# Optimization experiments

Hardware: AMD Instinct MI355X
Metric: run time of the kernel (lower is better)

## Reference

```python
import jax, jax.numpy as jnp
import numpy as np

B, T, D = 128, 1024, 128

def setup_inputs() -> dict:
    key = jax.random.key(0)
    k1, k2 = jax.random.split(key)
    x = jax.random.normal(k1, (B, T, 3 * D), dtype=jnp.float32)
    # original init: kernel = gain * eye(d_dim); use eye plus small noise for a nontrivial test
    kernel = jnp.eye(D, dtype=jnp.float32) + 0.01 * jax.random.normal(k2, (D, D), dtype=jnp.float32)
    return {"x": x, "kernel": kernel}

def reference(x, kernel):
    d = kernel.shape[0]
    # x: (B, T, 3d) -> channel blocks (module permutes to (B,C,T) then back; net effect is slicing last dim)
    y = x[:, :, :d]            # (B, T, d) observed values
    w = x[:, :, d:2 * d]       # (B, T, d) log-intensities
    y_obs = x[:, :, 2 * d:3 * d]  # (B, T, d) transient targets
    intensity = jnp.exp(w)
    # softmax across channels per timestep (exp(w - logsumexp_d w))
    sm = jax.nn.softmax(w, axis=2)
    mean = jnp.mean(y, axis=1, keepdims=True)  # (B, 1, d), broadcast over T
    # cross-channel mixing: small per-timestep d x d matmul
    smooth = jnp.matmul(sm * (y - mean), kernel) + mean  # (B, T, d)
    y_trans = y_obs - smooth
    # concat order matches torch.cat([rep1, intensity, y_trans], dim=1) after final permute
    return jnp.concatenate([smooth, intensity, y_trans], axis=-1)  # (B, T, 3d)
```

## Files before the change

### kernel.cpp

```cpp
#include <hip/hip_runtime.h>
#include <cstdint>

#define D_CH 128
#define T_LEN 1024
#define ROWLEN 384
#define NROWS (128 * 1024)
#define TILE 64
#define NCHUNK (NROWS / TILE)
#define VSTR_B 272
#define VS_SLICE (16 * VSTR_B)
#define EPI_W 132
#define EPI_SLICE (16 * EPI_W * 4)

typedef __attribute__((ext_vector_type(8))) _Float16 f16x8;
typedef __attribute__((ext_vector_type(4))) _Float16 f16x4;
typedef __attribute__((ext_vector_type(4))) float f32x4;

__global__ __launch_bounds__(256) void prep_kernel(const float* __restrict__ x,
                                                   const float* __restrict__ Kmat,
                                                   float* __restrict__ meang,
                                                   _Float16* __restrict__ Ktg) {
  int bid = blockIdx.x;
  int b = bid >> 1, h = bid & 1;
  int tid = threadIdx.x;
  int li = tid & 15, tt = tid >> 4;
  int d4 = h * 64 + 4 * li;
  float4 s = make_float4(0.f, 0.f, 0.f, 0.f);
  const float* xp = x + (size_t)b * T_LEN * ROWLEN + d4;
#pragma unroll 4
  for (int j = 0; j < 64; ++j) {
    int t = tt + 16 * j;
    float4 v = *(const float4*)(xp + (size_t)t * ROWLEN);
    s.x += v.x; s.y += v.y; s.z += v.z; s.w += v.w;
  }
  __shared__ float4 red[16][17];
  red[tt][li] = s;
  __syncthreads();
  for (int st = 8; st > 0; st >>= 1) {
    if (tt < st) {
      float4 o = red[tt + st][li];
      float4 m = red[tt][li];
      m.x += o.x; m.y += o.y; m.z += o.z; m.w += o.w;
      red[tt][li] = m;
    }
    __syncthreads();
  }
  if (tt == 0) {
    float4 m = red[0][li];
    const float inv = 1.0f / 1024.0f;
    m.x *= inv; m.y *= inv; m.z *= inv; m.w *= inv;
    *(float4*)(meang + b * D_CH + d4) = m;
  }
  if (tid < 64) {
    int f = bid * 64 + tid;
    int j = f & 7;
    int lane = (f >> 3) & 63;
    int q = f >> 9;
    int ks = q & 3, nt = q >> 2;
    int kk = ks * 32 + (lane >> 4) * 8 + j;
    int nn = nt * 16 + (lane & 15);
    Ktg[f] = (_Float16)Kmat[kk * D_CH + nn];
  }
}

__global__ __launch_bounds__(256, 3) void main_kernel(const float* __restrict__ x,
                                                      const float* __restrict__ meang,
                                                      const _Float16* __restrict__ Ktg,
                                                      float* __restrict__ out) {
  __shared__ alignas(16) char vsbuf[4 * VS_SLICE];
  __shared__ alignas(16) char epibuf[4 * EPI_SLICE];
  int tid = threadIdx.x;
  int wave = tid >> 6, lane = tid & 63;
  int hf = lane >> 5, li = lane & 31;
  int c0 = 4 * li;
  int m0 = wave * 16;
  int l15 = lane & 15, lg = lane >> 4;
  char* vslice = vsbuf + wave * VS_SLICE;
  float* epi = (float*)(epibuf + wave * EPI_SLICE);

  int chunk = blockIdx.x;
  int row0 = chunk * TILE;
  int bb = chunk >> 4;
  const float* mb = meang + bb * D_CH;
  float4 mn = *(const float4*)(mb + c0);

  float4 yb[8], wb[8];
#pragma unroll
  for (int i = 0; i < 8; ++i) {
    size_t base = (size_t)(row0 + m0 + 2 * i + hf) * ROWLEN + c0;
    yb[i] = *(const float4*)(x + base);
    wb[i] = *(const float4*)(x + base + 128);
  }
#pragma unroll
  for (int i = 0; i < 8; ++i) {
    int lr = 2 * i + hf;
    int row = row0 + m0 + lr;
    float4 e;
    e.x = __expf(wb[i].x); e.y = __expf(wb[i].y);
    e.z = __expf(wb[i].z); e.w = __expf(wb[i].w);
    *(float4*)(out + (size_t)row * ROWLEN + 128 + c0) = e;
    float s = e.x + e.y + e.z + e.w;
    s += __shfl_xor(s, 1, 32);
    s += __shfl_xor(s, 2, 32);
    s += __shfl_xor(s, 4, 32);
    s += __shfl_xor(s, 8, 32);
    s += __shfl_xor(s, 16, 32);
    float rinv = 1.0f / s;
    f16x4 vh;
    vh[0] = (_Float16)(e.x * rinv * (yb[i].x - mn.x));
    vh[1] = (_Float16)(e.y * rinv * (yb[i].y - mn.y));
    vh[2] = (_Float16)(e.z * rinv * (yb[i].z - mn.z));
    vh[3] = (_Float16)(e.w * rinv * (yb[i].w - mn.w));
    *(f16x4*)(vslice + lr * VSTR_B + li * 8) = vh;
  }

  f16x8 a[4];
#pragma unroll
  for (int ks = 0; ks < 4; ++ks)
    a[ks] = *(const f16x8*)(vslice + l15 * VSTR_B + ks * 64 + lg * 16);
  f32x4 acc[8];
#pragma unroll
  for (int nt = 0; nt < 8; ++nt) {
    acc[nt] = (f32x4){0.f, 0.f, 0.f, 0.f};
#pragma unroll
    for (int ks = 0; ks < 4; ++ks) {
      f16x8 bf = *(const f16x8*)&Ktg[((nt * 4 + ks) * 64 + lane) * 8];
      acc[nt] = __builtin_amdgcn_mfma_f32_16x16x32_f16(a[ks], bf, acc[nt], 0, 0, 0);
    }
  }

#pragma unroll
  for (int nt = 0; nt < 8; ++nt)
#pragma unroll
    for (int r = 0; r < 4; ++r)
      epi[(lg * 4 + r) * EPI_W + nt * 16 + l15] = acc[nt][r];

#pragma unroll
  for (int i = 0; i < 8; ++i) {
    int lr = 2 * i + hf;
    size_t ob = (size_t)(row0 + m0 + lr) * ROWLEN;
    float4 sm4 = *(const float4*)&epi[lr * EPI_W + c0];
    sm4.x += mn.x; sm4.y += mn.y; sm4.z += mn.z; sm4.w += mn.w;
    float4 yo = *(const float4*)(x + ob + 256 + c0);
    *(float4*)(out + ob + c0) = sm4;
    float4 yt;
    yt.x = yo.x - sm4.x; yt.y = yo.y - sm4.y;
    yt.z = yo.z - sm4.z; yt.w = yo.w - sm4.w;
    *(float4*)(out + ob + 256 + c0) = yt;
  }
}

extern "C" void kernel_launch(void* const* d_in, const int* in_sizes, int n_in,
                              void* d_out, int out_size, void* d_ws, size_t ws_size,
                              hipStream_t stream) {
  const float* x = (const float*)d_in[0];
  const float* Kmat = (const float*)d_in[1];
  float* out = (float*)d_out;
  float* meang = (float*)d_ws;
  _Float16* Ktg = (_Float16*)((char*)d_ws + 65536);
  prep_kernel<<<256, 256, 0, stream>>>(x, Kmat, meang, Ktg);
  main_kernel<<<NCHUNK, 256, 0, stream>>>(x, meang, Ktg, out);
}
```

Baseline: 350.2 us.

## Alias LDS buffers, use nontemporal global access, widen prep reduction blocks

The main kernel now reuses one per-wave LDS slice for both the fp16 MFMA operand staging and the fp32 epilogue buffer. This cuts shared memory per block, and the launch bound goes from 3 to 4 blocks per CU to take advantage of it. All streaming loads of x and stores to out use nontemporal builtins, to avoid polluting the cache with data that is touched only once. The prep kernel moves to 1024 threads per block with a deeper tree reduction, so each thread does fewer serial loads for the mean. The aliasing relies on in-wave LDS ordering, since there is no barrier between the last operand read and the first epilogue write.

```diff
diff --git a/kernel.cpp b/kernel.cpp
--- a/kernel.cpp
+++ b/kernel.cpp
@@ -8,48 +8,40 @@
 #define TILE 64
 #define NCHUNK (NROWS / TILE)
 #define VSTR_B 272
-#define VS_SLICE (16 * VSTR_B)
 #define EPI_W 132
-#define EPI_SLICE (16 * EPI_W * 4)
+#define SLICE_B 8448
 
 typedef __attribute__((ext_vector_type(8))) _Float16 f16x8;
 typedef __attribute__((ext_vector_type(4))) _Float16 f16x4;
 typedef __attribute__((ext_vector_type(4))) float f32x4;
 
-__global__ __launch_bounds__(256) void prep_kernel(const float* __restrict__ x,
-                                                   const float* __restrict__ Kmat,
-                                                   float* __restrict__ meang,
-                                                   _Float16* __restrict__ Ktg) {
+__global__ __launch_bounds__(1024) void prep_kernel(const float* __restrict__ x,
+                                                    const float* __restrict__ Kmat,
+                                                    float* __restrict__ meang,
+                                                    _Float16* __restrict__ Ktg) {
   int bid = blockIdx.x;
   int b = bid >> 1, h = bid & 1;
   int tid = threadIdx.x;
   int li = tid & 15, tt = tid >> 4;
   int d4 = h * 64 + 4 * li;
-  float4 s = make_float4(0.f, 0.f, 0.f, 0.f);
+  f32x4 s = {0.f, 0.f, 0.f, 0.f};
   const float* xp = x + (size_t)b * T_LEN * ROWLEN + d4;
 #pragma unroll 4
-  for (int j = 0; j < 64; ++j) {
-    int t = tt + 16 * j;
-    float4 v = *(const float4*)(xp + (size_t)t * ROWLEN);
-    s.x += v.x; s.y += v.y; s.z += v.z; s.w += v.w;
+  for (int j = 0; j < 16; ++j) {
+    int t = tt + 64 * j;
+    f32x4 v = *(const f32x4*)(xp + (size_t)t * ROWLEN);
+    s += v;
   }
-  __shared__ float4 red[16][17];
+  __shared__ f32x4 red[64][17];
   red[tt][li] = s;
   __syncthreads();
-  for (int st = 8; st > 0; st >>= 1) {
-    if (tt < st) {
-      float4 o = red[tt + st][li];
-      float4 m = red[tt][li];
-      m.x += o.x; m.y += o.y; m.z += o.z; m.w += o.w;
-      red[tt][li] = m;
-    }
+  for (int st = 32; st > 0; st >>= 1) {
+    if (tt < st) red[tt][li] += red[tt + st][li];
     __syncthreads();
   }
   if (tt == 0) {
-    float4 m = red[0][li];
-    const float inv = 1.0f / 1024.0f;
-    m.x *= inv; m.y *= inv; m.z *= inv; m.w *= inv;
-    *(float4*)(meang + b * D_CH + d4) = m;
+    f32x4 m = red[0][li] * (1.0f / 1024.0f);
+    *(f32x4*)(meang + b * D_CH + d4) = m;
   }
   if (tid < 64) {
     int f = bid * 64 + tid;
@@ -63,43 +55,42 @@
   }
 }
 
-__global__ __launch_bounds__(256, 3) void main_kernel(const float* __restrict__ x,
+__global__ __launch_bounds__(256, 4) void main_kernel(const float* __restrict__ x,
                                                       const float* __restrict__ meang,
                                                       const _Float16* __restrict__ Ktg,
                                                       float* __restrict__ out) {
-  __shared__ alignas(16) char vsbuf[4 * VS_SLICE];
-  __shared__ alignas(16) char epibuf[4 * EPI_SLICE];
+  __shared__ alignas(16) char smem[4 * SLICE_B];
   int tid = threadIdx.x;
   int wave = tid >> 6, lane = tid & 63;
   int hf = lane >> 5, li = lane & 31;
   int c0 = 4 * li;
   int m0 = wave * 16;
   int l15 = lane & 15, lg = lane >> 4;
-  char* vslice = vsbuf + wave * VS_SLICE;
-  float* epi = (float*)(epibuf + wave * EPI_SLICE);
+  char* vslice = smem + wave * SLICE_B;
+  float* epi = (float*)(smem + wave * SLICE_B);
 
   int chunk = blockIdx.x;
   int row0 = chunk * TILE;
   int bb = chunk >> 4;
   const float* mb = meang + bb * D_CH;
-  float4 mn = *(const float4*)(mb + c0);
+  f32x4 mn = *(const f32x4*)(mb + c0);
 
-  float4 yb[8], wb[8];
+  f32x4 yb[8], wb[8];
 #pragma unroll
   for (int i = 0; i < 8; ++i) {
     size_t base = (size_t)(row0 + m0 + 2 * i + hf) * ROWLEN + c0;
-    yb[i] = *(const float4*)(x + base);
-    wb[i] = *(const float4*)(x + base + 128);
+    yb[i] = __builtin_nontemporal_load((const f32x4*)(x + base));
+    wb[i] = __builtin_nontemporal_load((const f32x4*)(x + base + 128));
   }
 #pragma unroll
   for (int i = 0; i < 8; ++i) {
     int lr = 2 * i + hf;
     int row = row0 + m0 + lr;
-    float4 e;
-    e.x = __expf(wb[i].x); e.y = __expf(wb[i].y);
-    e.z = __expf(wb[i].z); e.w = __expf(wb[i].w);
-    *(float4*)(out + (size_t)row * ROWLEN + 128 + c0) = e;
-    float s = e.x + e.y + e.z + e.w;
+    f32x4 e;
+    e[0] = __expf(wb[i][0]); e[1] = __expf(wb[i][1]);
+    e[2] = __expf(wb[i][2]); e[3] = __expf(wb[i][3]);
+    __builtin_nontemporal_store(e, (f32x4*)(out + (size_t)row * ROWLEN + 128 + c0));
+    float s = e[0] + e[1] + e[2] + e[3];
     s += __shfl_xor(s, 1, 32);
     s += __shfl_xor(s, 2, 32);
     s += __shfl_xor(s, 4, 32);
@@ -107,10 +98,10 @@
     s += __shfl_xor(s, 16, 32);
     float rinv = 1.0f / s;
     f16x4 vh;
-    vh[0] = (_Float16)(e.x * rinv * (yb[i].x - mn.x));
-    vh[1] = (_Float16)(e.y * rinv * (yb[i].y - mn.y));
-    vh[2] = (_Float16)(e.z * rinv * (yb[i].z - mn.z));
-    vh[3] = (_Float16)(e.w * rinv * (yb[i].w - mn.w));
+    vh[0] = (_Float16)(e[0] * rinv * (yb[i][0] - mn[0]));
+    vh[1] = (_Float16)(e[1] * rinv * (yb[i][1] - mn[1]));
+    vh[2] = (_Float16)(e[2] * rinv * (yb[i][2] - mn[2]));
+    vh[3] = (_Float16)(e[3] * rinv * (yb[i][3] - mn[3]));
     *(f16x4*)(vslice + lr * VSTR_B + li * 8) = vh;
   }
 
@@ -139,14 +130,12 @@
   for (int i = 0; i < 8; ++i) {
     int lr = 2 * i + hf;
     size_t ob = (size_t)(row0 + m0 + lr) * ROWLEN;
-    float4 sm4 = *(const float4*)&epi[lr * EPI_W + c0];
-    sm4.x += mn.x; sm4.y += mn.y; sm4.z += mn.z; sm4.w += mn.w;
-    float4 yo = *(const float4*)(x + ob + 256 + c0);
-    *(float4*)(out + ob + c0) = sm4;
-    float4 yt;
-    yt.x = yo.x - sm4.x; yt.y = yo.y - sm4.y;
-    yt.z = yo.z - sm4.z; yt.w = yo.w - sm4.w;
-    *(float4*)(out + ob + 256 + c0) = yt;
+    f32x4 sm4 = *(const f32x4*)&epi[lr * EPI_W + c0];
+    sm4 += mn;
+    f32x4 yo = __builtin_nontemporal_load((const f32x4*)(x + ob + 256 + c0));
+    __builtin_nontemporal_store(sm4, (f32x4*)(out + ob + c0));
+    f32x4 yt = yo - sm4;
+    __builtin_nontemporal_store(yt, (f32x4*)(out + ob + 256 + c0));
   }
 }
 
@@ -158,6 +147,6 @@
   float* out = (float*)d_out;
   float* meang = (float*)d_ws;
   _Float16* Ktg = (_Float16*)((char*)d_ws + 65536);
-  prep_kernel<<<256, 256, 0, stream>>>(x, Kmat, meang, Ktg);
+  prep_kernel<<<256, 1024, 0, stream>>>(x, Kmat, meang, Ktg);
   main_kernel<<<NCHUNK, 256, 0, stream>>>(x, meang, Ktg, out);
 }
```

Result: no change. 343.8 us (-1.8%).
